# Kernel tuning notes

Measured on AMD Instinct MI355X. Metric: run time of the kernel, lower is better.

The kernel has to match this reference:

```python
import jax, jax.numpy as jnp
import numpy as np

NUM_CLASSES = 81
THRESH_HI = 0.5
THRESH_LO = 0.4
GAMMA = 2.0
ALPHA = 0.25
VARIANCE = (0.1, 0.2)  # cfg['variance'] in ssd.pytorch
B, P, T = 32, 24564, 20


def setup_inputs() -> dict:
    key = jax.random.key(0)
    k1, k2, k3, k4, k5, k6, k7 = jax.random.split(key, 7)
    loc_data = jax.random.normal(k1, (B, P, 4), jnp.float32)
    conf_data = jax.random.normal(k2, (B, P, NUM_CLASSES), jnp.float32)
    # priors in center form (cx, cy, w, h), all in [0,1]
    pcxy = jax.random.uniform(k3, (P, 2), minval=0.05, maxval=0.95)
    pwh = jax.random.uniform(k4, (P, 2), minval=0.04, maxval=0.5)
    priors = jnp.concatenate([pcxy, pwh], axis=-1).astype(jnp.float32)
    # ground-truth boxes in point form (xmin, ymin, xmax, ymax) + label
    tcxy = jax.random.uniform(k5, (B, T, 2), minval=0.1, maxval=0.9)
    twh = jax.random.uniform(k6, (B, T, 2), minval=0.05, maxval=0.4)
    boxes = jnp.clip(jnp.concatenate([tcxy - twh / 2, tcxy + twh / 2], -1), 0.0, 1.0)
    labels = jax.random.randint(k7, (B, T), 0, NUM_CLASSES - 1).astype(jnp.float32)
    targets = jnp.concatenate([boxes, labels[..., None]], axis=-1)  # [B,T,5]
    return {"loc_data": loc_data, "conf_data": conf_data, "priors": priors, "targets": targets}


def point_form(pr):
    # center form -> (xmin,ymin,xmax,ymax)
    return jnp.concatenate([pr[:, :2] - pr[:, 2:] / 2, pr[:, :2] + pr[:, 2:] / 2], -1)


def jaccard(box_a, box_b):
    # box_a [T,4], box_b [P,4], both point form -> IoU [T,P]
    lt = jnp.maximum(box_a[:, None, :2], box_b[None, :, :2])
    rb = jnp.minimum(box_a[:, None, 2:], box_b[None, :, 2:])
    wh = jnp.clip(rb - lt, 0.0)
    inter = wh[..., 0] * wh[..., 1]
    area_a = ((box_a[:, 2] - box_a[:, 0]) * (box_a[:, 3] - box_a[:, 1]))[:, None]
    area_b = ((box_b[:, 2] - box_b[:, 0]) * (box_b[:, 3] - box_b[:, 1]))[None, :]
    return inter / (area_a + area_b - inter)


def encode(matched, priors):
    # matched [P,4] point form, priors [P,4] center form
    g_cxcy = ((matched[:, :2] + matched[:, 2:]) / 2 - priors[:, :2]) / (VARIANCE[0] * priors[:, 2:])
    g_wh = jnp.log((matched[:, 2:] - matched[:, :2]) / priors[:, 2:]) / VARIANCE[1]
    return jnp.concatenate([g_cxcy, g_wh], -1)


def match_one(truths, labels, priors):
    # truths [T,4] point form, labels [T], priors [P,4] center form
    ov = jaccard(truths, point_form(priors))          # [T,P]
    best_prior_idx = jnp.argmax(ov, axis=1)           # [T] best prior per gt
    best_truth_overlap = jnp.max(ov, axis=0)          # [P]
    best_truth_idx = jnp.argmax(ov, axis=0)           # [P]
    # ensure every gt box keeps its best prior
    best_truth_overlap = best_truth_overlap.at[best_prior_idx].set(2.0)
    best_truth_idx = best_truth_idx.at[best_prior_idx].set(jnp.arange(truths.shape[0]))
    matched = truths[best_truth_idx]                  # [P,4]
    conf = labels[best_truth_idx].astype(jnp.int32) + 1
    conf = jnp.where(best_truth_overlap < THRESH_HI, -1, conf)  # ignore band
    conf = jnp.where(best_truth_overlap < THRESH_LO, 0, conf)   # background
    return encode(matched, priors), conf


def reference(loc_data, conf_data, priors, targets):
    truths = targets[..., :4]
    labels = targets[..., 4]
    loc_t, conf_t = jax.vmap(lambda t, l: match_one(t, l, priors))(truths, labels)
    pos = conf_t > 0                                  # [B,P]
    # smooth L1 over positive priors (sum reduction)
    diff = loc_data - loc_t
    ad = jnp.abs(diff)
    sl1 = jnp.where(ad < 1.0, 0.5 * diff * diff, ad - 0.5)
    loss_l = jnp.sum(sl1 * pos[..., None])
    # focal loss over ALL locations (ignore conf==-1)
    logits = conf_data.reshape(-1, NUM_CLASSES)
    tgt = conf_t.reshape(-1)
    valid = tgt >= 0
    tgt_safe = jnp.where(valid, tgt, 0)
    logpt = jnp.take_along_axis(jax.nn.log_softmax(logits, -1), tgt_safe[:, None], 1)[:, 0]
    pt = jnp.exp(logpt)
    alpha_t = jnp.where(tgt > 0, ALPHA, 1.0 - ALPHA)
    fl = -alpha_t * (1.0 - pt) ** GAMMA * logpt
    loss_c = jnp.sum(jnp.where(valid, fl, 0.0))
    n = jnp.sum(pos).astype(loc_data.dtype)
    return loss_l / n, loss_c / n
```

## Files before the change

kernel.cpp:

```cpp
#include <hip/hip_runtime.h>

#define NCLS 81
#define BB 32
#define PP 24564
#define TT 20
#define KM_BLOCKS_X 96
#define KL_BLOCKS 2048
#define KL_ROWS 64
#define KL_CHUNKS ((BB * PP) / KL_ROWS)
#define KL_F4 ((KL_ROWS * NCLS) / 4)

#define GLOAD_LDS16(g, l)                                                  \
    __builtin_amdgcn_global_load_lds(                                      \
        (const __attribute__((address_space(1))) void*)(g),                \
        (__attribute__((address_space(3))) void*)(l), 16, 0, 0)

__device__ __forceinline__ float iou_rn(float tx1, float ty1, float tx2, float ty2, float ta,
                                        float X1, float Y1, float X2, float Y2, float pa)
{
    float lx = fmaxf(tx1, X1);
    float ly = fmaxf(ty1, Y1);
    float rx = fminf(tx2, X2);
    float ry = fminf(ty2, Y2);
    float w = fmaxf(__fsub_rn(rx, lx), 0.0f);
    float h = fmaxf(__fsub_rn(ry, ly), 0.0f);
    float inter = __fmul_rn(w, h);
    float denom = __fsub_rn(__fadd_rn(ta, pa), inter);
    return __fdiv_rn(inter, denom);
}

__global__ __launch_bounds__(1024)
void k_best_prior(const float* __restrict__ priors,
                  const float* __restrict__ targets,
                  unsigned long long* __restrict__ bp)
{
    const int t = blockIdx.x;
    const int b = blockIdx.y;
    const float* tb = targets + (b * TT + t) * 5;
    const float tx1 = tb[0], ty1 = tb[1], tx2 = tb[2], ty2 = tb[3];
    const float ta = __fmul_rn(__fsub_rn(tx2, tx1), __fsub_rn(ty2, ty1));

    unsigned long long best = 0ull;
    for (int p = threadIdx.x; p < PP; p += 1024) {
        float px = priors[p * 4 + 0], py = priors[p * 4 + 1];
        float pw = priors[p * 4 + 2], ph = priors[p * 4 + 3];
        float hw = __fmul_rn(pw, 0.5f), hh = __fmul_rn(ph, 0.5f);
        float X1 = __fsub_rn(px, hw), Y1 = __fsub_rn(py, hh);
        float X2 = __fadd_rn(px, hw), Y2 = __fadd_rn(py, hh);
        float pa = __fmul_rn(__fsub_rn(X2, X1), __fsub_rn(Y2, Y1));
        float ov = iou_rn(tx1, ty1, tx2, ty2, ta, X1, Y1, X2, Y2, pa);
        unsigned long long pk = ((unsigned long long)__float_as_uint(ov) << 32)
                              | (unsigned long long)(0xFFFFFFFFu - (unsigned)p);
        if (pk > best) best = pk;
    }

    #pragma unroll
    for (int s = 32; s; s >>= 1) {
        unsigned long long o = __shfl_xor(best, s, 64);
        if (o > best) best = o;
    }
    __shared__ unsigned long long wred[16];
    if ((threadIdx.x & 63) == 0) wred[threadIdx.x >> 6] = best;
    __syncthreads();
    if (threadIdx.x == 0) {
        unsigned long long b2 = wred[0];
        #pragma unroll
        for (int w = 1; w < 16; ++w) if (wred[w] > b2) b2 = wred[w];
        bp[b * TT + t] = b2;
    }
}

__global__ __launch_bounds__(256)
void k_match(const float* __restrict__ loc,
             const float* __restrict__ priors,
             const float* __restrict__ targets,
             const unsigned long long* __restrict__ bp,
             unsigned char* __restrict__ code,
             float* __restrict__ pl, float* __restrict__ pn)
{
    const int b = blockIdx.y;
    const int p = blockIdx.x * 256 + threadIdx.x;

    __shared__ float trb[TT * 5];
    __shared__ unsigned int bpb[TT];
    if (threadIdx.x < TT * 5) trb[threadIdx.x] = targets[b * TT * 5 + threadIdx.x];
    if (threadIdx.x < TT)
        bpb[threadIdx.x] = 0xFFFFFFFFu - (unsigned)(bp[b * TT + threadIdx.x] & 0xFFFFFFFFull);
    __syncthreads();

    float accL = 0.0f, accN = 0.0f;

    if (p < PP) {
        float px = priors[p * 4 + 0], py = priors[p * 4 + 1];
        float pw = priors[p * 4 + 2], ph = priors[p * 4 + 3];
        float hw = __fmul_rn(pw, 0.5f), hh = __fmul_rn(ph, 0.5f);
        float X1 = __fsub_rn(px, hw), Y1 = __fsub_rn(py, hh);
        float X2 = __fadd_rn(px, hw), Y2 = __fadd_rn(py, hh);
        float pa = __fmul_rn(__fsub_rn(X2, X1), __fsub_rn(Y2, Y1));

        float bI = -1.0f, bD = 1.0f;
        int bt = 0;
        #pragma unroll
        for (int t = 0; t < TT; ++t) {
            float tx1 = trb[t * 5 + 0], ty1 = trb[t * 5 + 1];
            float tx2 = trb[t * 5 + 2], ty2 = trb[t * 5 + 3];
            float ta2 = __fmul_rn(__fsub_rn(tx2, tx1), __fsub_rn(ty2, ty1));
            float lx = fmaxf(tx1, X1), ly = fmaxf(ty1, Y1);
            float rx = fminf(tx2, X2), ry = fminf(ty2, Y2);
            float w = fmaxf(__fsub_rn(rx, lx), 0.0f);
            float h = fmaxf(__fsub_rn(ry, ly), 0.0f);
            float inter = __fmul_rn(w, h);
            float denom = __fsub_rn(__fadd_rn(ta2, pa), inter);
            if (__fmul_rn(inter, bD) > __fmul_rn(bI, denom)) { bI = inter; bD = denom; bt = t; }
        }
        float bov = __fdiv_rn(bI, bD);

        bool forced = false;
        #pragma unroll
        for (int t = 0; t < TT; ++t) {
            if (bpb[t] == (unsigned)p) { bt = t; forced = true; }
        }
        if (forced) bov = 2.0f;

        int c = (int)trb[bt * 5 + 4] + 1;
        if (bov < 0.5f) c = -1;
        if (bov < 0.4f) c = 0;

        const int r = b * PP + p;
        code[r] = (unsigned char)(c + 1);

        if (c > 0) {
            float mx1 = trb[bt * 5 + 0], my1 = trb[bt * 5 + 1];
            float mx2 = trb[bt * 5 + 2], my2 = trb[bt * 5 + 3];
            float cx = __fmul_rn(__fadd_rn(mx1, mx2), 0.5f);
            float cy = __fmul_rn(__fadd_rn(my1, my2), 0.5f);
            float gx = __fdiv_rn(__fsub_rn(cx, px), __fmul_rn(0.1f, pw));
            float gy = __fdiv_rn(__fsub_rn(cy, py), __fmul_rn(0.1f, ph));
            float gw = __fdiv_rn(logf(__fdiv_rn(__fsub_rn(mx2, mx1), pw)), 0.2f);
            float gh = __fdiv_rn(logf(__fdiv_rn(__fsub_rn(my2, my1), ph)), 0.2f);
            const float* ld = loc + (size_t)r * 4;
            float g0 = ld[0] - gx, g1 = ld[1] - gy, g2 = ld[2] - gw, g3 = ld[3] - gh;
            float a0 = fabsf(g0), a1 = fabsf(g1), a2 = fabsf(g2), a3 = fabsf(g3);
            accL += (a0 < 1.0f) ? 0.5f * g0 * g0 : (a0 - 0.5f);
            accL += (a1 < 1.0f) ? 0.5f * g1 * g1 : (a1 - 0.5f);
            accL += (a2 < 1.0f) ? 0.5f * g2 * g2 : (a2 - 0.5f);
            accL += (a3 < 1.0f) ? 0.5f * g3 * g3 : (a3 - 0.5f);
            accN += 1.0f;
        }
    }

    __shared__ float red[256];
    red[threadIdx.x] = accL;
    __syncthreads();
    for (int s = 128; s; s >>= 1) {
        if (threadIdx.x < s) red[threadIdx.x] += red[threadIdx.x + s];
        __syncthreads();
    }
    if (threadIdx.x == 0) pl[blockIdx.y * KM_BLOCKS_X + blockIdx.x] = red[0];
    __syncthreads();

    red[threadIdx.x] = accN;
    __syncthreads();
    for (int s = 128; s; s >>= 1) {
        if (threadIdx.x < s) red[threadIdx.x] += red[threadIdx.x + s];
        __syncthreads();
    }
    if (threadIdx.x == 0) pn[blockIdx.y * KM_BLOCKS_X + blockIdx.x] = red[0];
}

__global__ __launch_bounds__(256)
void k_loss(const float* __restrict__ conf,
            const unsigned char* __restrict__ code,
            float* __restrict__ pc)
{
    __shared__ float buf[2][KL_ROWS * NCLS];

    const int tid = threadIdx.x;
    const int w = tid >> 6;
    const int lane = tid & 63;
    const int rl = tid >> 2;
    const int k = tid & 3;
    const float4* conf4 = (const float4*)conf;

    auto stage = [&](int c, int buf_idx) {
        const float4* src = conf4 + (size_t)c * KL_F4;
        float4* dst = (float4*)buf[buf_idx];
        #pragma unroll
        for (int j = 0; j < 5; ++j) {
            int idx = j * 256 + w * 64 + lane;
            GLOAD_LDS16(src + idx, dst + idx);
        }
        if (w == 0 && lane < 16) {
            int idx = 1280 + lane;
            GLOAD_LDS16(src + idx, dst + idx);
        }
    };

    const int c0 = blockIdx.x;
    stage(c0, 0);
    __syncthreads();

    float accC = 0.0f;
    int cur = 0;

    for (int c = c0; c < KL_CHUNKS; c += KL_BLOCKS) {
        int cn = c + KL_BLOCKS;
        if (cn < KL_CHUNKS) stage(cn, cur ^ 1);

        const float* row = buf[cur] + rl * NCLS;
        float se = 0.0f;
        #pragma unroll
        for (int i = 0; i < 20; ++i) se += __expf(row[k * 20 + i]);
        if (k == 0) se += __expf(row[80]);
        se += __shfl_xor(se, 1, 4);
        se += __shfl_xor(se, 2, 4);

        if (k == 0) {
            int r = c * KL_ROWS + rl;
            int cc = (int)code[r] - 1;
            if (cc >= 0) {
                float xt = row[cc];
                float logpt = xt - __logf(se);
                float pt = __expf(logpt);
                float at = (cc > 0) ? 0.25f : 0.75f;
                float om = 1.0f - pt;
                accC -= at * om * om * logpt;
            }
        }
        __syncthreads();
        cur ^= 1;
    }

    __shared__ float red[256];
    red[tid] = accC;
    __syncthreads();
    for (int s = 128; s; s >>= 1) {
        if (tid < s) red[tid] += red[tid + s];
        __syncthreads();
    }
    if (tid == 0) pc[blockIdx.x] = red[0];
}

__global__ __launch_bounds__(256)
void k_final(const float* __restrict__ pl, const float* __restrict__ pn,
             const float* __restrict__ pc, float* __restrict__ out)
{
    __shared__ float sl[256], sc[256], sn[256];
    float L = 0.0f, C = 0.0f, N = 0.0f;
    for (int i = threadIdx.x; i < BB * KM_BLOCKS_X; i += 256) { L += pl[i]; N += pn[i]; }
    for (int i = threadIdx.x; i < KL_BLOCKS; i += 256) C += pc[i];
    sl[threadIdx.x] = L; sc[threadIdx.x] = C; sn[threadIdx.x] = N;
    __syncthreads();
    for (int s = 128; s; s >>= 1) {
        if (threadIdx.x < s) {
            sl[threadIdx.x] += sl[threadIdx.x + s];
            sc[threadIdx.x] += sc[threadIdx.x + s];
            sn[threadIdx.x] += sn[threadIdx.x + s];
        }
        __syncthreads();
    }
    if (threadIdx.x == 0) {
        out[0] = sl[0] / sn[0];
        out[1] = sc[0] / sn[0];
    }
}

extern "C" void kernel_launch(void* const* d_in, const int* in_sizes, int n_in,
                              void* d_out, int out_size, void* d_ws, size_t ws_size,
                              hipStream_t stream)
{
    const float* loc     = (const float*)d_in[0];
    const float* conf    = (const float*)d_in[1];
    const float* priors  = (const float*)d_in[2];
    const float* targets = (const float*)d_in[3];
    float* out = (float*)d_out;

    char* ws = (char*)d_ws;
    unsigned long long* bp = (unsigned long long*)ws;
    unsigned char* code = (unsigned char*)(ws + 4096);
    float* pl = (float*)(ws + 4096 + 790528);
    float* pn = pl + BB * KM_BLOCKS_X;
    float* pc = pn + BB * KM_BLOCKS_X;

    k_best_prior<<<dim3(TT, BB), 1024, 0, stream>>>(priors, targets, bp);
    k_match<<<dim3(KM_BLOCKS_X, BB), 256, 0, stream>>>(loc, priors, targets, bp, code, pl, pn);
    k_loss<<<KL_BLOCKS, 256, 0, stream>>>(conf, code, pc);
    k_final<<<1, 256, 0, stream>>>(pl, pn, pc, out);
}
```

Measured before the change: 84.06 us.

## Segment best-prior search across targets and shrink focal-loss chunk rows

The best-prior kernel now gives each block a segment of priors and loops over all 20 targets. Each prior is loaded and converted once, not once per target, and per-segment maxima are written out. The match kernel then reduces these partial maxima. The loss kernel moves to 32-row chunks with 8 threads per row and 1792 blocks, trading smaller LDS tiles and more shuffle steps for better occupancy and finer work distribution.

After: 85.32 us. No clear change (+1.5%).

```diff
diff --git a/kernel.cpp b/kernel.cpp
--- a/kernel.cpp
+++ b/kernel.cpp
@@ -5,8 +5,10 @@
 #define PP 24564
 #define TT 20
 #define KM_BLOCKS_X 96
-#define KL_BLOCKS 2048
-#define KL_ROWS 64
+#define BP_SEGS 8
+#define BP_SEG 3072
+#define KL_BLOCKS 1792
+#define KL_ROWS 32
 #define KL_CHUNKS ((BB * PP) / KL_ROWS)
 #define KL_F4 ((KL_ROWS * NCLS) / 4)
 
@@ -15,58 +17,69 @@
         (const __attribute__((address_space(1))) void*)(g),                \
         (__attribute__((address_space(3))) void*)(l), 16, 0, 0)
 
-__device__ __forceinline__ float iou_rn(float tx1, float ty1, float tx2, float ty2, float ta,
-                                        float X1, float Y1, float X2, float Y2, float pa)
-{
-    float lx = fmaxf(tx1, X1);
-    float ly = fmaxf(ty1, Y1);
-    float rx = fminf(tx2, X2);
-    float ry = fminf(ty2, Y2);
-    float w = fmaxf(__fsub_rn(rx, lx), 0.0f);
-    float h = fmaxf(__fsub_rn(ry, ly), 0.0f);
-    float inter = __fmul_rn(w, h);
-    float denom = __fsub_rn(__fadd_rn(ta, pa), inter);
-    return __fdiv_rn(inter, denom);
-}
-
 __global__ __launch_bounds__(1024)
-void k_best_prior(const float* __restrict__ priors,
-                  const float* __restrict__ targets,
-                  unsigned long long* __restrict__ bp)
-{
-    const int t = blockIdx.x;
+void k_bp(const float* __restrict__ priors,
+          const float* __restrict__ targets,
+          unsigned long long* __restrict__ bp_part)
+{
+    const int seg = blockIdx.x;
     const int b = blockIdx.y;
-    const float* tb = targets + (b * TT + t) * 5;
-    const float tx1 = tb[0], ty1 = tb[1], tx2 = tb[2], ty2 = tb[3];
-    const float ta = __fmul_rn(__fsub_rn(tx2, tx1), __fsub_rn(ty2, ty1));
-
-    unsigned long long best = 0ull;
-    for (int p = threadIdx.x; p < PP; p += 1024) {
-        float px = priors[p * 4 + 0], py = priors[p * 4 + 1];
-        float pw = priors[p * 4 + 2], ph = priors[p * 4 + 3];
-        float hw = __fmul_rn(pw, 0.5f), hh = __fmul_rn(ph, 0.5f);
-        float X1 = __fsub_rn(px, hw), Y1 = __fsub_rn(py, hh);
-        float X2 = __fadd_rn(px, hw), Y2 = __fadd_rn(py, hh);
-        float pa = __fmul_rn(__fsub_rn(X2, X1), __fsub_rn(Y2, Y1));
-        float ov = iou_rn(tx1, ty1, tx2, ty2, ta, X1, Y1, X2, Y2, pa);
-        unsigned long long pk = ((unsigned long long)__float_as_uint(ov) << 32)
-                              | (unsigned long long)(0xFFFFFFFFu - (unsigned)p);
-        if (pk > best) best = pk;
-    }
-
+
+    __shared__ float trb[TT * 5];
+    __shared__ unsigned long long wred[TT][16];
+    if (threadIdx.x < TT * 5) trb[threadIdx.x] = targets[b * TT * 5 + threadIdx.x];
+    __syncthreads();
+
+    float X1[3], Y1[3], X2[3], Y2[3], pa[3];
+    unsigned int pkey[3];
+    bool ok[3];
     #pragma unroll
-    for (int s = 32; s; s >>= 1) {
-        unsigned long long o = __shfl_xor(best, s, 64);
-        if (o > best) best = o;
-    }
-    __shared__ unsigned long long wred[16];
-    if ((threadIdx.x & 63) == 0) wred[threadIdx.x >> 6] = best;
-    __syncthreads();
-    if (threadIdx.x == 0) {
-        unsigned long long b2 = wred[0];
-        #pragma unroll
-        for (int w = 1; w < 16; ++w) if (wred[w] > b2) b2 = wred[w];
-        bp[b * TT + t] = b2;
+    for (int j = 0; j < 3; ++j) {
+        int p = seg * BP_SEG + j * 1024 + threadIdx.x;
+        ok[j] = p < PP;
+        float4 pr = ok[j] ? ((const float4*)priors)[p] : make_float4(1.f, 1.f, 0.f, 0.f);
+        float hw = __fmul_rn(pr.z, 0.5f), hh = __fmul_rn(pr.w, 0.5f);
+        X1[j] = __fsub_rn(pr.x, hw); Y1[j] = __fsub_rn(pr.y, hh);
+        X2[j] = __fadd_rn(pr.x, hw); Y2[j] = __fadd_rn(pr.y, hh);
+        pa[j] = __fmul_rn(__fsub_rn(X2[j], X1[j]), __fsub_rn(Y2[j], Y1[j]));
+        pkey[j] = 0xFFFFFFFFu - (unsigned)p;
+    }
+
+    const int wv = threadIdx.x >> 6;
+    const int lane = threadIdx.x & 63;
+
+    for (int t = 0; t < TT; ++t) {
+        float tx1 = trb[t * 5 + 0], ty1 = trb[t * 5 + 1];
+        float tx2 = trb[t * 5 + 2], ty2 = trb[t * 5 + 3];
+        float ta = __fmul_rn(__fsub_rn(tx2, tx1), __fsub_rn(ty2, ty1));
+
+        unsigned long long best = 0ull;
+        #pragma unroll
+        for (int j = 0; j < 3; ++j) {
+            float lx = fmaxf(tx1, X1[j]), ly = fmaxf(ty1, Y1[j]);
+            float rx = fminf(tx2, X2[j]), ry = fminf(ty2, Y2[j]);
+            float w = fmaxf(__fsub_rn(rx, lx), 0.0f);
+            float h = fmaxf(__fsub_rn(ry, ly), 0.0f);
+            float inter = __fmul_rn(w, h);
+            float denom = __fsub_rn(__fadd_rn(ta, pa[j]), inter);
+            float ov = __fdiv_rn(inter, denom);
+            unsigned long long key = ok[j]
+                ? (((unsigned long long)__float_as_uint(ov) << 32) | pkey[j]) : 0ull;
+            if (key > best) best = key;
+        }
+        #pragma unroll
+        for (int s = 32; s; s >>= 1) {
+            unsigned long long o = __shfl_xor(best, s, 64);
+            if (o > best) best = o;
+        }
+        if (lane == 0) wred[t][wv] = best;
+    }
+    __syncthreads();
+    if (threadIdx.x < TT) {
+        unsigned long long m = wred[threadIdx.x][0];
+        #pragma unroll
+        for (int w = 1; w < 16; ++w) if (wred[threadIdx.x][w] > m) m = wred[threadIdx.x][w];
+        bp_part[(b * TT + threadIdx.x) * BP_SEGS + seg] = m;
     }
 }
 
@@ -74,7 +87,7 @@
 void k_match(const float* __restrict__ loc,
              const float* __restrict__ priors,
              const float* __restrict__ targets,
-             const unsigned long long* __restrict__ bp,
+             const unsigned long long* __restrict__ bp_part,
              unsigned char* __restrict__ code,
              float* __restrict__ pl, float* __restrict__ pn)
 {
@@ -84,8 +97,13 @@
     __shared__ float trb[TT * 5];
     __shared__ unsigned int bpb[TT];
     if (threadIdx.x < TT * 5) trb[threadIdx.x] = targets[b * TT * 5 + threadIdx.x];
-    if (threadIdx.x < TT)
-        bpb[threadIdx.x] = 0xFFFFFFFFu - (unsigned)(bp[b * TT + threadIdx.x] & 0xFFFFFFFFull);
+    if (threadIdx.x < TT) {
+        const unsigned long long* q = bp_part + (b * TT + threadIdx.x) * BP_SEGS;
+        unsigned long long m = q[0];
+        #pragma unroll
+        for (int s = 1; s < BP_SEGS; ++s) if (q[s] > m) m = q[s];
+        bpb[threadIdx.x] = 0xFFFFFFFFu - (unsigned)(m & 0xFFFFFFFFull);
+    }
     __syncthreads();
 
     float accL = 0.0f, accN = 0.0f;
@@ -178,20 +196,20 @@
     const int tid = threadIdx.x;
     const int w = tid >> 6;
     const int lane = tid & 63;
-    const int rl = tid >> 2;
-    const int k = tid & 3;
+    const int rl = tid >> 3;
+    const int k = tid & 7;
     const float4* conf4 = (const float4*)conf;
 
     auto stage = [&](int c, int buf_idx) {
         const float4* src = conf4 + (size_t)c * KL_F4;
         float4* dst = (float4*)buf[buf_idx];
         #pragma unroll
-        for (int j = 0; j < 5; ++j) {
+        for (int j = 0; j < 2; ++j) {
             int idx = j * 256 + w * 64 + lane;
             GLOAD_LDS16(src + idx, dst + idx);
         }
-        if (w == 0 && lane < 16) {
-            int idx = 1280 + lane;
+        if (tid < KL_F4 - 512) {
+            int idx = 512 + w * 64 + lane;
             GLOAD_LDS16(src + idx, dst + idx);
         }
     };
@@ -210,10 +228,11 @@
         const float* row = buf[cur] + rl * NCLS;
         float se = 0.0f;
         #pragma unroll
-        for (int i = 0; i < 20; ++i) se += __expf(row[k * 20 + i]);
+        for (int i = 0; i < 10; ++i) se += __expf(row[k * 10 + i]);
         if (k == 0) se += __expf(row[80]);
-        se += __shfl_xor(se, 1, 4);
-        se += __shfl_xor(se, 2, 4);
+        se += __shfl_xor(se, 1, 8);
+        se += __shfl_xor(se, 2, 8);
+        se += __shfl_xor(se, 4, 8);
 
         if (k == 0) {
             int r = c * KL_ROWS + rl;
@@ -276,14 +295,14 @@
     float* out = (float*)d_out;
 
     char* ws = (char*)d_ws;
-    unsigned long long* bp = (unsigned long long*)ws;
-    unsigned char* code = (unsigned char*)(ws + 4096);
-    float* pl = (float*)(ws + 4096 + 790528);
+    unsigned long long* bp_part = (unsigned long long*)ws;
+    unsigned char* code = (unsigned char*)(ws + 65536);
+    float* pl = (float*)(ws + 65536 + 790528);
     float* pn = pl + BB * KM_BLOCKS_X;
     float* pc = pn + BB * KM_BLOCKS_X;
 
-    k_best_prior<<<dim3(TT, BB), 1024, 0, stream>>>(priors, targets, bp);
-    k_match<<<dim3(KM_BLOCKS_X, BB), 256, 0, stream>>>(loc, priors, targets, bp, code, pl, pn);
+    k_bp<<<dim3(BP_SEGS, BB), 1024, 0, stream>>>(priors, targets, bp_part);
+    k_match<<<dim3(KM_BLOCKS_X, BB), 256, 0, stream>>>(loc, priors, targets, bp_part, code, pl, pn);
     k_loss<<<KL_BLOCKS, 256, 0, stream>>>(conf, code, pc);
     k_final<<<1, 256, 0, stream>>>(pl, pn, pc, out);
 }
```
